# Kernel optimization log

Measured on AMD Instinct MI355X. Metric: run time of the kernel, lower is better.

The kernel has to match this reference:

```python
import jax, jax.numpy as jnp
import numpy as np

BS, N, D, B, D_PM = 8, 4096, 1024, 8, 64
BUDGET = 16.0


def setup_inputs() -> dict:
    key = jax.random.key(0)
    ks = jax.random.split(key, 6)
    H = jax.random.normal(ks[0], (BS, N, D), jnp.float32)
    surprise = jax.random.normal(ks[1], (BS, N, D), jnp.float32)
    # W_pm initialized as (1/B)*I + small noise, as in initialize()
    eye = jnp.eye(D_PM, dtype=jnp.float32)
    W_pm = eye / B + 0.01 * jax.random.normal(ks[2], (BS, B, D_PM, D_PM), jnp.float32)
    proj_in_w = jax.random.normal(ks[3], (D_PM, D), jnp.float32) / np.float32(np.sqrt(D))
    proj_in_b = jnp.zeros((D_PM,), jnp.float32)
    # original zero-inits proj_out; use small values so output is non-trivial
    proj_out_w = 0.02 * jax.random.normal(ks[4], (D, D_PM), jnp.float32)
    proj_out_b = jnp.zeros((D,), jnp.float32)
    raw_beta = jnp.full((B,), -3.0, jnp.float32)
    raw_decay = jnp.full((B,), np.float32(np.log(0.999 / 0.001)), jnp.float32)  # logit(0.999)
    surp_scale = jnp.ones((1,), jnp.float32)
    surp_bias = jnp.zeros((1,), jnp.float32)
    return dict(H=H, surprise=surprise, W_pm=W_pm,
                proj_in_w=proj_in_w, proj_in_b=proj_in_b,
                proj_out_w=proj_out_w, proj_out_b=proj_out_b,
                raw_beta=raw_beta, raw_decay=raw_decay,
                surp_scale=surp_scale, surp_bias=surp_bias)


def reference(H, surprise, W_pm, proj_in_w, proj_in_b, proj_out_w, proj_out_b,
              raw_beta, raw_decay, surp_scale, surp_bias):
    # ---- read ----
    pre = jnp.einsum('bnd,pd->bnp', H, proj_in_w) + proj_in_b          # [BS,N,D_pm]
    W_sum = jnp.sum(W_pm, axis=1)                                      # [BS,D_pm,D_pm]
    post = jnp.einsum('bnp,bqp->bnq', pre, W_sum)                      # pre @ W_sum^T
    pm_read = jnp.einsum('bnq,dq->bnd', post, proj_out_w) + proj_out_b # [BS,N,D]
    # ---- commit (Hebbian, surprise-gated) ----
    surp_mag = jnp.linalg.norm(surprise, axis=-1)                      # [BS,N]
    s = jax.nn.sigmoid(surp_scale * surp_mag + surp_bias)              # [BS,N]
    weighted = jnp.sqrt(s)[..., None] * pre                            # [BS,N,D_pm]
    G = jnp.einsum('bnp,bnq->bpq', weighted, weighted) / N             # [BS,D_pm,D_pm]
    beta = jax.nn.softplus(raw_beta)                                   # [B]
    decay = jax.nn.sigmoid(raw_decay)                                  # [B]
    eye = jnp.eye(D_PM, dtype=pre.dtype)
    T = decay[None, :, None, None] * eye + beta[None, :, None, None] * G[:, None]  # [BS,B,D_pm,D_pm]
    W_new = jnp.einsum('bkij,bkjq->bkiq', W_pm, T)                     # [BS,B,D_pm,D_pm]
    frob = jnp.sqrt(jnp.sum(W_new * W_new, axis=(-2, -1), keepdims=True))
    scale = jnp.minimum(BUDGET / jnp.maximum(frob, 1e-8), 1.0)
    W_new = W_new * scale
    return pm_read, W_new
```

## Files before the change

kernel.cpp:

```cpp
#include <hip/hip_runtime.h>

typedef unsigned short u16;
typedef unsigned int u32;
typedef __attribute__((ext_vector_type(4))) float f32x4;
typedef __attribute__((ext_vector_type(8))) short s16x8;

static constexpr int N_ = 4096;
static constexpr int D_ = 1024;

#define WAITV(N) asm volatile("s_waitcnt vmcnt(" #N ")" ::: "memory")
#define MEMCLOB() asm volatile("" ::: "memory")

__device__ __forceinline__ u16 f2bf(float f) {
  unsigned u = __float_as_uint(f);
  u += 0x7FFFu + ((u >> 16) & 1u);
  return (u16)(u >> 16);
}

__device__ __forceinline__ f32x4 zero4() {
  f32x4 z; z[0] = 0.f; z[1] = 0.f; z[2] = 0.f; z[3] = 0.f; return z;
}

__device__ __forceinline__ void gload16(const void* g, void* lds) {
  __builtin_amdgcn_global_load_lds(
      (const __attribute__((address_space(1))) u32*)g,
      (__attribute__((address_space(3))) u32*)lds, 16, 0, 0);
}

__global__ __launch_bounds__(256) void k_aux(
    const float* __restrict__ Wpm, const float* __restrict__ piw,
    const float* __restrict__ pw, const float* __restrict__ Sur,
    const float* __restrict__ sscale_p, const float* __restrict__ sbias_p,
    u16* __restrict__ WpB, u16* __restrict__ MB, float* __restrict__ sqs_ws) {
  __shared__ float Ws[64][65];
  int bid = blockIdx.x, tid = threadIdx.x;
  if (bid < 16) {
    size_t i0 = (size_t)bid * 4096;
    for (int idx = tid; idx < 4096; idx += 256)
      WpB[i0 + idx] = f2bf(piw[i0 + idx]);
    return;
  }
  if (bid < 144) {
    int idx2 = bid - 16;
    int b = idx2 >> 4, t = idx2 & 15;
    for (int idx = tid; idx < 4096; idx += 256) {
      float s = 0.f;
#pragma unroll
      for (int k = 0; k < 8; ++k)
        s += Wpm[((size_t)(b * 8 + k)) * 4096 + idx];
      Ws[idx >> 6][idx & 63] = s;
    }
    __syncthreads();
    u16* mb = MB + ((size_t)b << 16);
    for (int oidx = tid; oidx < 4096; oidx += 256) {
      int r = oidx >> 6, c = oidx & 63;
      int drow = t * 64 + r;
      const float* prow = pw + (size_t)drow * 64;
      float acc = 0.f;
#pragma unroll 8
      for (int q = 0; q < 64; ++q) acc += prow[q] * Ws[q][c];
      mb[(size_t)drow * 64 + c] = f2bf(acc);
    }
    return;
  }
  int w = tid >> 6, lane = tid & 63;
  int fr = (bid - 144) * 16 + w * 4;
  const float4* r0 = (const float4*)(Sur + (size_t)fr * 1024) + lane;
  float s0 = 0.f, s1 = 0.f, s2 = 0.f, s3 = 0.f;
#pragma unroll
  for (int c = 0; c < 4; ++c) {
    float4 v0 = r0[c * 64];
    float4 v1 = r0[256 + c * 64];
    float4 v2 = r0[512 + c * 64];
    float4 v3 = r0[768 + c * 64];
    s0 += v0.x * v0.x + v0.y * v0.y + v0.z * v0.z + v0.w * v0.w;
    s1 += v1.x * v1.x + v1.y * v1.y + v1.z * v1.z + v1.w * v1.w;
    s2 += v2.x * v2.x + v2.y * v2.y + v2.z * v2.z + v2.w * v2.w;
    s3 += v3.x * v3.x + v3.y * v3.y + v3.z * v3.z + v3.w * v3.w;
  }
#pragma unroll
  for (int m = 1; m < 64; m <<= 1) {
    s0 += __shfl_xor(s0, m, 64);
    s1 += __shfl_xor(s1, m, 64);
    s2 += __shfl_xor(s2, m, 64);
    s3 += __shfl_xor(s3, m, 64);
  }
  float res = s0;
  if (lane == 1) res = s1;
  if (lane == 2) res = s2;
  if (lane == 3) res = s3;
  if (lane < 4) {
    float mag = sqrtf(res);
    float s = 1.f / (1.f + __expf(-(sscale_p[0] * mag + sbias_p[0])));
    sqs_ws[fr + lane] = sqrtf(s);
  }
}

__global__ __launch_bounds__(512, 4) void k_main(
    const float* __restrict__ H, const float* __restrict__ pib,
    const float* __restrict__ pob, const u16* __restrict__ WpB,
    const u16* __restrict__ MB, const float* __restrict__ sqs_ws,
    float* __restrict__ Gpart, float* __restrict__ out) {
  __shared__ __align__(16) char arena[32768];
  __shared__ __align__(16) u16 preRP[64][72];
  __shared__ __align__(16) u16 wRPT[64][72];
  __shared__ float pobL[1024];

  const int tid = threadIdx.x;
  const int lane = tid & 63;
  const int w = tid >> 6;
  const int wm = w & 3;
  const int wk = w >> 2;
  const int llo = lane & 15;
  const int lhi = lane >> 4;
  const int b = blockIdx.x >> 6;
  const int row0 = (blockIdx.x & 63) * 64;

  float bias_t[4];
#pragma unroll
  for (int t = 0; t < 4; ++t) bias_t[t] = pib[t * 16 + llo];
  float sqs_r[4];
#pragma unroll
  for (int r = 0; r < 4; ++r)
    sqs_r[r] = sqs_ws[b * 4096 + row0 + wm * 16 + lhi * 4 + r];

  const int srow = 8 * w + (lane >> 3);
  const int sc16 = (lane & 7) ^ (srow & 7);

  f32x4 accA[4];
#pragma unroll
  for (int t = 0; t < 4; ++t) accA[t] = zero4();

  const float* hsrc = H + ((size_t)b * N_ + row0 + srow) * D_ + sc16 * 4;
  const u16* wpb = WpB + (size_t)wk * 512 + lhi * 8;

  s16x8 B0[4], B1[4];
  auto LOADB = [&](int kc, s16x8* Bs) {
#pragma unroll
    for (int t = 0; t < 4; ++t)
      Bs[t] = *(const s16x8*)(wpb + (size_t)(t * 16 + llo) * 1024 + kc * 32);
  };
  auto STAGEH = [&](int kc, int buf) {
    gload16(hsrc + kc * 32, arena + buf * 16384 + w * 1024);
    gload16(hsrc + 512 + kc * 32, arena + buf * 16384 + 8192 + w * 1024);
  };
  const int arow = wm * 16 + llo;
  const int r7a = arow & 7;
  auto COMPA = [&](int buf, const s16x8* Bs) {
    const char* abase = arena + buf * 16384 + wk * 8192 + arow * 128;
    f32x4 alo = *(const f32x4*)(abase + (((lhi * 2) ^ r7a) * 16));
    f32x4 ahi = *(const f32x4*)(abase + (((lhi * 2 + 1) ^ r7a) * 16));
    s16x8 af;
    af[0] = (short)f2bf(alo[0]); af[1] = (short)f2bf(alo[1]);
    af[2] = (short)f2bf(alo[2]); af[3] = (short)f2bf(alo[3]);
    af[4] = (short)f2bf(ahi[0]); af[5] = (short)f2bf(ahi[1]);
    af[6] = (short)f2bf(ahi[2]); af[7] = (short)f2bf(ahi[3]);
#pragma unroll
    for (int t = 0; t < 4; ++t)
      accA[t] = __builtin_amdgcn_mfma_f32_16x16x32_bf16(af, Bs[t], accA[t], 0, 0, 0);
  };

  LOADB(0, B0); STAGEH(0, 0);
  MEMCLOB();
  LOADB(1, B1); STAGEH(1, 1);
  MEMCLOB();

  for (int kc = 0; kc < 16; kc += 2) {
    WAITV(6);
    __builtin_amdgcn_s_barrier();
    COMPA(0, B0);
    MEMCLOB();
    __builtin_amdgcn_s_barrier();
    if (kc + 2 < 16) { LOADB(kc + 2, B0); STAGEH(kc + 2, 0); }
    MEMCLOB();
    if (kc + 1 == 15) { WAITV(0); } else { WAITV(6); }
    __builtin_amdgcn_s_barrier();
    COMPA(1, B1);
    MEMCLOB();
    __builtin_amdgcn_s_barrier();
    if (kc + 3 < 16) { LOADB(kc + 3, B1); STAGEH(kc + 3, 1); }
    MEMCLOB();
  }

  __syncthreads();
  float (*preF)[65] = (float(*)[65])arena;
  if (wk == 1) {
#pragma unroll
    for (int t = 0; t < 4; ++t)
#pragma unroll
      for (int r = 0; r < 4; ++r)
        preF[wm * 16 + lhi * 4 + r][t * 16 + llo] = accA[t][r];
  }
  __syncthreads();
  if (wk == 0) {
#pragma unroll
    for (int t = 0; t < 4; ++t)
#pragma unroll
      for (int r = 0; r < 4; ++r) {
        int row = wm * 16 + lhi * 4 + r;
        float v = accA[t][r] + preF[row][t * 16 + llo] + bias_t[t];
        preRP[row][t * 16 + llo] = f2bf(v);
        wRPT[t * 16 + llo][row] = f2bf(v * sqs_r[r]);
      }
  }
  __syncthreads();

  {
    f32x4 accG[4];
#pragma unroll
    for (int t = 0; t < 4; ++t) accG[t] = zero4();
    s16x8 ag = *(const s16x8*)&wRPT[wm * 16 + llo][wk * 32 + lhi * 8];
#pragma unroll
    for (int t = 0; t < 4; ++t) {
      s16x8 bg = *(const s16x8*)&wRPT[t * 16 + llo][wk * 32 + lhi * 8];
      accG[t] = __builtin_amdgcn_mfma_f32_16x16x32_bf16(ag, bg, accG[t], 0, 0, 0);
    }
    float* gout = Gpart + ((size_t)blockIdx.x * 2 + wk) * 4096;
#pragma unroll
    for (int t = 0; t < 4; ++t)
#pragma unroll
      for (int r = 0; r < 4; ++r)
        gout[(wm * 16 + lhi * 4 + r) * 64 + t * 16 + llo] = accG[t][r];
  }

  pobL[tid] = pob[tid];
  pobL[tid + 512] = pob[tid + 512];
  __syncthreads();

  const u16* mbb = MB + ((size_t)b << 16);
  const u16* msrc0 = mbb + (size_t)srow * 64 + sc16 * 8;
  auto STAGED = [&](int c, int buf) {
    gload16(msrc0 + (size_t)c * 64 * 64, arena + buf * 16384 + w * 1024);
    gload16(msrc0 + (size_t)(512 + c * 64) * 64, arena + buf * 16384 + 8192 + w * 1024);
  };
  s16x8 ad0 = *(const s16x8*)&preRP[wm * 16 + llo][lhi * 8];
  s16x8 ad1 = *(const s16x8*)&preRP[wm * 16 + llo][32 + lhi * 8];
  float* orow = out + ((size_t)b * N_ + row0 + wm * 16) * D_;

  STAGED(0, 0);
  MEMCLOB();
  STAGED(1, 1);
  MEMCLOB();
  for (int c = 0; c < 8; ++c) {
    if (c == 0) { WAITV(2); }
    else if (c == 7) { WAITV(16); }
    else { WAITV(18); }
    __builtin_amdgcn_s_barrier();
    {
      const char* dbase = arena + (c & 1) * 16384 + wk * 8192;
#pragma unroll
      for (int i = 0; i < 4; ++i) {
        int row = i * 16 + llo;
        int r7 = row & 7;
        const char* base = dbase + row * 128;
        s16x8 b0 = *(const s16x8*)(base + ((lhi ^ r7) * 16));
        s16x8 b1 = *(const s16x8*)(base + (((4 + lhi) ^ r7) * 16));
        f32x4 acc = zero4();
        acc = __builtin_amdgcn_mfma_f32_16x16x32_bf16(ad0, b0, acc, 0, 0, 0);
        acc = __builtin_amdgcn_mfma_f32_16x16x32_bf16(ad1, b1, acc, 0, 0, 0);
        int n0 = wk * 512 + c * 64 + i * 16;
        float bias = pobL[n0 + llo];
#pragma unroll
        for (int r = 0; r < 4; ++r)
          orow[(size_t)(lhi * 4 + r) * D_ + n0 + llo] = acc[r] + bias;
      }
    }
    MEMCLOB();
    __builtin_amdgcn_s_barrier();
    if (c + 2 < 8) STAGED(c + 2, c & 1);
    MEMCLOB();
  }
}

__global__ __launch_bounds__(256) void k_wnew(
    const float* __restrict__ Wpm, const float* __restrict__ Gpart,
    const float* __restrict__ rbeta, const float* __restrict__ rdecay,
    float* __restrict__ outW) {
  __shared__ float Wk[64][68];
  __shared__ float Gl[64][68];
  __shared__ float red[4];
  int bk = blockIdx.x;
  int b = bk >> 3, k = bk & 7;
  int tid = threadIdx.x;
  f32x4 a0 = zero4(), a1 = zero4(), a2 = zero4(), a3 = zero4();
  const float* gp = Gpart + (size_t)b * 128 * 4096 + tid * 16;
#pragma unroll 2
  for (int sl = 0; sl < 128; ++sl) {
    const f32x4* p = (const f32x4*)(gp + (size_t)sl * 4096);
    a0 += p[0]; a1 += p[1]; a2 += p[2]; a3 += p[3];
  }
  {
    float* gl = &Gl[tid >> 2][(tid & 3) * 16];
#pragma unroll
    for (int j = 0; j < 4; ++j) {
      gl[j] = a0[j]; gl[4 + j] = a1[j]; gl[8 + j] = a2[j]; gl[12 + j] = a3[j];
    }
  }
  const float* wsrc = Wpm + (size_t)bk * 4096;
  for (int idx = tid; idx < 4096; idx += 256)
    Wk[idx >> 6][idx & 63] = wsrc[idx];
  __syncthreads();
  float beta = log1pf(__expf(rbeta[k]));
  float decay = 1.f / (1.f + __expf(-rdecay[k]));
  float bn = beta * (1.f / 4096.f);
  int q = tid & 63;
  int rbase = tid >> 6;
  float vals[16];
  float ss = 0.f;
#pragma unroll
  for (int i = 0; i < 16; ++i) {
    int row = i * 4 + rbase;
    float acc = 0.f;
#pragma unroll 8
    for (int j = 0; j < 64; ++j) acc += Wk[row][j] * Gl[j][q];
    float v = decay * Wk[row][q] + bn * acc;
    vals[i] = v;
    ss += v * v;
  }
#pragma unroll
  for (int m = 1; m < 64; m <<= 1) ss += __shfl_xor(ss, m, 64);
  if ((tid & 63) == 0) red[tid >> 6] = ss;
  __syncthreads();
  float frob = sqrtf(red[0] + red[1] + red[2] + red[3]);
  float scale = fminf(16.f / fmaxf(frob, 1e-8f), 1.f);
  float* dst = outW + (size_t)bk * 4096;
#pragma unroll
  for (int i = 0; i < 16; ++i) dst[i * 256 + tid] = vals[i] * scale;
}

extern "C" void kernel_launch(void* const* d_in, const int* in_sizes, int n_in,
                              void* d_out, int out_size, void* d_ws, size_t ws_size,
                              hipStream_t stream) {
  const float* H      = (const float*)d_in[0];
  const float* Sur    = (const float*)d_in[1];
  const float* Wpm    = (const float*)d_in[2];
  const float* piw    = (const float*)d_in[3];
  const float* pib    = (const float*)d_in[4];
  const float* pw     = (const float*)d_in[5];
  const float* pob    = (const float*)d_in[6];
  const float* rbeta  = (const float*)d_in[7];
  const float* rdecay = (const float*)d_in[8];
  const float* sscale = (const float*)d_in[9];
  const float* sbias  = (const float*)d_in[10];
  float* out = (float*)d_out;

  char* ws = (char*)d_ws;
  u16* WpB      = (u16*)(ws);
  u16* MB       = (u16*)(ws + 131072);
  float* sqs_ws = (float*)(ws + 1179648);
  float* Gpart  = (float*)(ws + 1310720);

  k_aux<<<2192, 256, 0, stream>>>(Wpm, piw, pw, Sur, sscale, sbias,
                                  WpB, MB, sqs_ws);
  k_main<<<512, 512, 0, stream>>>(H, pib, pob, WpB, MB, sqs_ws, Gpart, out);
  k_wnew<<<64, 256, 0, stream>>>(Wpm, Gpart, rbeta, rdecay,
                                 out + (size_t)8 * 4096 * 1024);
}
```

Before: 162.3 us.

## Fuse surprise-norm into main kernel and split Gpart reduction into parallel kernel

Moves the per-row surprise norm and sigmoid gating from the aux kernel into the main GEMM loop. The surprise loads are interleaved with the H staging pipeline, so the aux kernel shrinks to 144 blocks and the sqs workspace round-trip goes away. Adds a separate 512-block kernel that reduces the 128 G partials per batch in parallel, replacing the serial 128-slice sum inside the 64-block k_wnew. The cost is more registers and memory traffic inside k_main, plus an extra kernel launch.

Result: faster. 140.4 us (-13.5%).

```diff
diff --git a/kernel.cpp b/kernel.cpp
--- a/kernel.cpp
+++ b/kernel.cpp
@@ -16,11 +16,9 @@
   u += 0x7FFFu + ((u >> 16) & 1u);
   return (u16)(u >> 16);
 }
-
 __device__ __forceinline__ f32x4 zero4() {
   f32x4 z; z[0] = 0.f; z[1] = 0.f; z[2] = 0.f; z[3] = 0.f; return z;
 }
-
 __device__ __forceinline__ void gload16(const void* g, void* lds) {
   __builtin_amdgcn_global_load_lds(
       (const __attribute__((address_space(1))) u32*)g,
@@ -29,9 +27,8 @@
 
 __global__ __launch_bounds__(256) void k_aux(
     const float* __restrict__ Wpm, const float* __restrict__ piw,
-    const float* __restrict__ pw, const float* __restrict__ Sur,
-    const float* __restrict__ sscale_p, const float* __restrict__ sbias_p,
-    u16* __restrict__ WpB, u16* __restrict__ MB, float* __restrict__ sqs_ws) {
+    const float* __restrict__ pw, u16* __restrict__ WpB,
+    u16* __restrict__ MB) {
   __shared__ float Ws[64][65];
   int bid = blockIdx.x, tid = threadIdx.x;
   if (bid < 16) {
@@ -40,71 +37,39 @@
       WpB[i0 + idx] = f2bf(piw[i0 + idx]);
     return;
   }
-  if (bid < 144) {
-    int idx2 = bid - 16;
-    int b = idx2 >> 4, t = idx2 & 15;
-    for (int idx = tid; idx < 4096; idx += 256) {
-      float s = 0.f;
-#pragma unroll
-      for (int k = 0; k < 8; ++k)
-        s += Wpm[((size_t)(b * 8 + k)) * 4096 + idx];
-      Ws[idx >> 6][idx & 63] = s;
-    }
-    __syncthreads();
-    u16* mb = MB + ((size_t)b << 16);
-    for (int oidx = tid; oidx < 4096; oidx += 256) {
-      int r = oidx >> 6, c = oidx & 63;
-      int drow = t * 64 + r;
-      const float* prow = pw + (size_t)drow * 64;
-      float acc = 0.f;
+  int idx2 = bid - 16;
+  int b = idx2 >> 4, t = idx2 & 15;
+  for (int idx = tid; idx < 4096; idx += 256) {
+    float s = 0.f;
+#pragma unroll
+    for (int k = 0; k < 8; ++k)
+      s += Wpm[((size_t)(b * 8 + k)) * 4096 + idx];
+    Ws[idx >> 6][idx & 63] = s;
+  }
+  __syncthreads();
+  u16* mb = MB + ((size_t)b << 16);
+  for (int oidx = tid; oidx < 4096; oidx += 256) {
+    int r = oidx >> 6, c = oidx & 63;
+    int drow = t * 64 + r;
+    const float* prow = pw + (size_t)drow * 64;
+    float acc = 0.f;
 #pragma unroll 8
-      for (int q = 0; q < 64; ++q) acc += prow[q] * Ws[q][c];
-      mb[(size_t)drow * 64 + c] = f2bf(acc);
-    }
-    return;
-  }
-  int w = tid >> 6, lane = tid & 63;
-  int fr = (bid - 144) * 16 + w * 4;
-  const float4* r0 = (const float4*)(Sur + (size_t)fr * 1024) + lane;
-  float s0 = 0.f, s1 = 0.f, s2 = 0.f, s3 = 0.f;
-#pragma unroll
-  for (int c = 0; c < 4; ++c) {
-    float4 v0 = r0[c * 64];
-    float4 v1 = r0[256 + c * 64];
-    float4 v2 = r0[512 + c * 64];
-    float4 v3 = r0[768 + c * 64];
-    s0 += v0.x * v0.x + v0.y * v0.y + v0.z * v0.z + v0.w * v0.w;
-    s1 += v1.x * v1.x + v1.y * v1.y + v1.z * v1.z + v1.w * v1.w;
-    s2 += v2.x * v2.x + v2.y * v2.y + v2.z * v2.z + v2.w * v2.w;
-    s3 += v3.x * v3.x + v3.y * v3.y + v3.z * v3.z + v3.w * v3.w;
-  }
-#pragma unroll
-  for (int m = 1; m < 64; m <<= 1) {
-    s0 += __shfl_xor(s0, m, 64);
-    s1 += __shfl_xor(s1, m, 64);
-    s2 += __shfl_xor(s2, m, 64);
-    s3 += __shfl_xor(s3, m, 64);
-  }
-  float res = s0;
-  if (lane == 1) res = s1;
-  if (lane == 2) res = s2;
-  if (lane == 3) res = s3;
-  if (lane < 4) {
-    float mag = sqrtf(res);
-    float s = 1.f / (1.f + __expf(-(sscale_p[0] * mag + sbias_p[0])));
-    sqs_ws[fr + lane] = sqrtf(s);
+    for (int q = 0; q < 64; ++q) acc += prow[q] * Ws[q][c];
+    mb[(size_t)drow * 64 + c] = f2bf(acc);
   }
 }
 
 __global__ __launch_bounds__(512, 4) void k_main(
-    const float* __restrict__ H, const float* __restrict__ pib,
-    const float* __restrict__ pob, const u16* __restrict__ WpB,
-    const u16* __restrict__ MB, const float* __restrict__ sqs_ws,
+    const float* __restrict__ H, const float* __restrict__ Sur,
+    const float* __restrict__ pib, const float* __restrict__ pob,
+    const float* __restrict__ sscale_p, const float* __restrict__ sbias_p,
+    const u16* __restrict__ WpB, const u16* __restrict__ MB,
     float* __restrict__ Gpart, float* __restrict__ out) {
   __shared__ __align__(16) char arena[32768];
   __shared__ __align__(16) u16 preRP[64][72];
   __shared__ __align__(16) u16 wRPT[64][72];
   __shared__ float pobL[1024];
+  __shared__ float sqsL[64];
 
   const int tid = threadIdx.x;
   const int lane = tid & 63;
@@ -119,22 +84,22 @@
   float bias_t[4];
 #pragma unroll
   for (int t = 0; t < 4; ++t) bias_t[t] = pib[t * 16 + llo];
-  float sqs_r[4];
-#pragma unroll
-  for (int r = 0; r < 4; ++r)
-    sqs_r[r] = sqs_ws[b * 4096 + row0 + wm * 16 + lhi * 4 + r];
+  const float sscale = sscale_p[0], sbias = sbias_p[0];
 
   const int srow = 8 * w + (lane >> 3);
   const int sc16 = (lane & 7) ^ (srow & 7);
-
-  f32x4 accA[4];
-#pragma unroll
-  for (int t = 0; t < 4; ++t) accA[t] = zero4();
-
   const float* hsrc = H + ((size_t)b * N_ + row0 + srow) * D_ + sc16 * 4;
   const u16* wpb = WpB + (size_t)wk * 512 + lhi * 8;
-
+  const float* surp =
+      Sur + ((size_t)b * N_ + row0 + (tid >> 3)) * D_ + (tid & 7) * 4;
+
+  f32x4 accA[4];
+#pragma unroll
+  for (int t = 0; t < 4; ++t) accA[t] = zero4();
   s16x8 B0[4], B1[4];
+  float4 surR0[2], surR1[2];
+  float ssq = 0.f;
+
   auto LOADB = [&](int kc, s16x8* Bs) {
 #pragma unroll
     for (int t = 0; t < 4; ++t)
@@ -162,24 +127,60 @@
 
   LOADB(0, B0); STAGEH(0, 0);
   MEMCLOB();
+  surR0[0] = *(const float4*)(surp);
+  surR0[1] = *(const float4*)(surp + 32);
+  MEMCLOB();
   LOADB(1, B1); STAGEH(1, 1);
   MEMCLOB();
+  surR1[0] = *(const float4*)(surp + 64);
+  surR1[1] = *(const float4*)(surp + 96);
+  MEMCLOB();
 
   for (int kc = 0; kc < 16; kc += 2) {
-    WAITV(6);
+    WAITV(8);
     __builtin_amdgcn_s_barrier();
     COMPA(0, B0);
-    MEMCLOB();
-    __builtin_amdgcn_s_barrier();
-    if (kc + 2 < 16) { LOADB(kc + 2, B0); STAGEH(kc + 2, 0); }
-    MEMCLOB();
-    if (kc + 1 == 15) { WAITV(0); } else { WAITV(6); }
+    ssq += surR0[0].x * surR0[0].x + surR0[0].y * surR0[0].y +
+           surR0[0].z * surR0[0].z + surR0[0].w * surR0[0].w +
+           surR0[1].x * surR0[1].x + surR0[1].y * surR0[1].y +
+           surR0[1].z * surR0[1].z + surR0[1].w * surR0[1].w;
+    MEMCLOB();
+    __builtin_amdgcn_s_barrier();
+    if (kc + 2 < 16) {
+      LOADB(kc + 2, B0); STAGEH(kc + 2, 0);
+      MEMCLOB();
+      surR0[0] = *(const float4*)(surp + (kc + 2) * 64);
+      surR0[1] = *(const float4*)(surp + (kc + 2) * 64 + 32);
+    }
+    MEMCLOB();
+    if (kc + 1 == 15) { WAITV(0); } else { WAITV(8); }
     __builtin_amdgcn_s_barrier();
     COMPA(1, B1);
-    MEMCLOB();
-    __builtin_amdgcn_s_barrier();
-    if (kc + 3 < 16) { LOADB(kc + 3, B1); STAGEH(kc + 3, 1); }
-    MEMCLOB();
+    ssq += surR1[0].x * surR1[0].x + surR1[0].y * surR1[0].y +
+           surR1[0].z * surR1[0].z + surR1[0].w * surR1[0].w +
+           surR1[1].x * surR1[1].x + surR1[1].y * surR1[1].y +
+           surR1[1].z * surR1[1].z + surR1[1].w * surR1[1].w;
+    MEMCLOB();
+    __builtin_amdgcn_s_barrier();
+    if (kc + 3 < 16) {
+      LOADB(kc + 3, B1); STAGEH(kc + 3, 1);
+      MEMCLOB();
+      surR1[0] = *(const float4*)(surp + (kc + 3) * 64);
+      surR1[1] = *(const float4*)(surp + (kc + 3) * 64 + 32);
+    }
+    MEMCLOB();
+  }
+
+  {
+    float a = ssq;
+    a += __shfl_xor(a, 1, 64);
+    a += __shfl_xor(a, 2, 64);
+    a += __shfl_xor(a, 4, 64);
+    if ((lane & 7) == 0) {
+      float mag = sqrtf(a);
+      float s = 1.f / (1.f + __expf(-(sscale * mag + sbias)));
+      sqsL[w * 8 + (lane >> 3)] = sqrtf(s);
+    }
   }
 
   __syncthreads();
@@ -193,6 +194,9 @@
   }
   __syncthreads();
   if (wk == 0) {
+    float sqs_r[4];
+#pragma unroll
+    for (int r = 0; r < 4; ++r) sqs_r[r] = sqsL[wm * 16 + lhi * 4 + r];
 #pragma unroll
     for (int t = 0; t < 4; ++t)
 #pragma unroll
@@ -222,7 +226,6 @@
       for (int r = 0; r < 4; ++r)
         gout[(wm * 16 + lhi * 4 + r) * 64 + t * 16 + llo] = accG[t][r];
   }
-
   pobL[tid] = pob[tid];
   pobL[tid + 512] = pob[tid + 512];
   __syncthreads();
@@ -272,33 +275,38 @@
   }
 }
 
+__global__ __launch_bounds__(256) void k_gred(
+    const float* __restrict__ Gpart, float* __restrict__ Gsum) {
+  __shared__ float red[4][64];
+  int b = blockIdx.x >> 6, g = blockIdx.x & 63;
+  int lane = threadIdx.x & 63, q = threadIdx.x >> 6;
+  const float* src = Gpart + ((size_t)b * 128 + q * 32) * 4096 + g * 64 + lane;
+  float s = 0.f;
+#pragma unroll 8
+  for (int i = 0; i < 32; ++i) s += src[(size_t)i * 4096];
+  red[q][lane] = s;
+  __syncthreads();
+  if (q == 0)
+    Gsum[(size_t)b * 4096 + g * 64 + lane] =
+        red[0][lane] + red[1][lane] + red[2][lane] + red[3][lane];
+}
+
 __global__ __launch_bounds__(256) void k_wnew(
-    const float* __restrict__ Wpm, const float* __restrict__ Gpart,
+    const float* __restrict__ Wpm, const float* __restrict__ Gsum,
     const float* __restrict__ rbeta, const float* __restrict__ rdecay,
     float* __restrict__ outW) {
-  __shared__ float Wk[64][68];
-  __shared__ float Gl[64][68];
+  __shared__ float Wk[64][66];
+  __shared__ float Gl[64][66];
   __shared__ float red[4];
   int bk = blockIdx.x;
   int b = bk >> 3, k = bk & 7;
   int tid = threadIdx.x;
-  f32x4 a0 = zero4(), a1 = zero4(), a2 = zero4(), a3 = zero4();
-  const float* gp = Gpart + (size_t)b * 128 * 4096 + tid * 16;
-#pragma unroll 2
-  for (int sl = 0; sl < 128; ++sl) {
-    const f32x4* p = (const f32x4*)(gp + (size_t)sl * 4096);
-    a0 += p[0]; a1 += p[1]; a2 += p[2]; a3 += p[3];
-  }
-  {
-    float* gl = &Gl[tid >> 2][(tid & 3) * 16];
-#pragma unroll
-    for (int j = 0; j < 4; ++j) {
-      gl[j] = a0[j]; gl[4 + j] = a1[j]; gl[8 + j] = a2[j]; gl[12 + j] = a3[j];
-    }
-  }
   const float* wsrc = Wpm + (size_t)bk * 4096;
-  for (int idx = tid; idx < 4096; idx += 256)
+  const float* gsrc = Gsum + (size_t)b * 4096;
+  for (int idx = tid; idx < 4096; idx += 256) {
     Wk[idx >> 6][idx & 63] = wsrc[idx];
+    Gl[idx >> 6][idx & 63] = gsrc[idx];
+  }
   __syncthreads();
   float beta = log1pf(__expf(rbeta[k]));
   float decay = 1.f / (1.f + __expf(-rdecay[k]));
@@ -345,14 +353,15 @@
   float* out = (float*)d_out;
 
   char* ws = (char*)d_ws;
-  u16* WpB      = (u16*)(ws);
-  u16* MB       = (u16*)(ws + 131072);
-  float* sqs_ws = (float*)(ws + 1179648);
-  float* Gpart  = (float*)(ws + 1310720);
-
-  k_aux<<<2192, 256, 0, stream>>>(Wpm, piw, pw, Sur, sscale, sbias,
-                                  WpB, MB, sqs_ws);
-  k_main<<<512, 512, 0, stream>>>(H, pib, pob, WpB, MB, sqs_ws, Gpart, out);
-  k_wnew<<<64, 256, 0, stream>>>(Wpm, Gpart, rbeta, rdecay,
+  u16* WpB     = (u16*)(ws);
+  u16* MB      = (u16*)(ws + 131072);
+  float* Gsum  = (float*)(ws + 1179648);
+  float* Gpart = (float*)(ws + 1310720);
+
+  k_aux<<<144, 256, 0, stream>>>(Wpm, piw, pw, WpB, MB);
+  k_main<<<512, 512, 0, stream>>>(H, Sur, pib, pob, sscale, sbias,
+                                  WpB, MB, Gpart, out);
+  k_gred<<<512, 256, 0, stream>>>(Gpart, Gsum);
+  k_wnew<<<64, 256, 0, stream>>>(Wpm, Gsum, rbeta, rdecay,
                                  out + (size_t)8 * 4096 * 1024);
 }
```
